# Optimization experiments

Hardware: AMD Instinct MI355X
Metric: run time of the kernel (lower is better)

The kernel has to match this reference:

```python
import jax, jax.numpy as jnp
import numpy as np

B, S, D = 2, 2048, 1024
H, DK, DV = 16, 64, 64
LN_EPS = 1e-5

def setup_inputs() -> dict:
    key = jax.random.key(0)
    ks = jax.random.split(key, 12)
    f = lambda k, shp: jax.random.normal(k, shp, dtype=jnp.float32)
    causal = jnp.triu(jnp.ones((S, S), dtype=jnp.bool_), k=1)  # True = masked
    return {
        'Q': f(ks[0], (B, S, D)),
        'K': f(ks[1], (B, S, D)),
        'V': f(ks[2], (B, S, D)),
        'attention_mask': jnp.broadcast_to(causal, (B, S, S)),
        'WQ_w': f(ks[3], (D, H * DK)) * 0.02, 'WQ_b': jnp.zeros((H * DK,), jnp.float32),
        'WK_w': f(ks[4], (D, H * DK)) * 0.02, 'WK_b': jnp.zeros((H * DK,), jnp.float32),
        'WV_w': f(ks[5], (H * DV, D)) * 0.02, 'WV_b': jnp.zeros((D,), jnp.float32),
        'lin_w': f(ks[6], (H * DV, D)) * 0.02, 'lin_b': jnp.zeros((D,), jnp.float32),
        'ln_g': jnp.ones((D,), jnp.float32), 'ln_b': jnp.zeros((D,), jnp.float32),
    }

def reference(Q, K, V, attention_mask, WQ_w, WQ_b, WK_w, WK_b, WV_w, WV_b, lin_w, lin_b, ln_g, ln_b):
    b = Q.shape[0]
    # projections -> (B, H, S, d)
    q = (Q @ WQ_w + WQ_b).reshape(b, -1, H, DK).transpose(0, 2, 1, 3)
    k = (K @ WK_w + WK_b).reshape(b, -1, H, DK).transpose(0, 2, 1, 3)
    v = (V @ WV_w + WV_b).reshape(b, -1, H, DV).transpose(0, 2, 1, 3)
    scale = 1.0 / jnp.sqrt(jnp.asarray(DK, Q.dtype))
    scores = jnp.einsum('bhqd,bhkd->bhqk', q, k) * scale  # (B,H,S,S)
    scores = jnp.where(attention_mask[:, None, :, :], -jnp.inf, scores)
    probs = jax.nn.softmax(scores, axis=-1)
    ctx = jnp.einsum('bhqk,bhkd->bhqd', probs, v)  # attention_weights in original
    ctx2 = ctx.transpose(0, 2, 1, 3).reshape(b, -1, H * DV)  # (B,S,H*DV)
    out = ctx2 @ lin_w + lin_b  # output projection
    res = out + Q
    mu = jnp.mean(res, axis=-1, keepdims=True)
    var = jnp.mean(jnp.square(res - mu), axis=-1, keepdims=True)
    y = (res - mu) * jax.lax.rsqrt(var + LN_EPS) * ln_g + ln_b
    return (y, ctx)
```

## Files before the change

### kernel.cpp

```cpp
#include <hip/hip_runtime.h>
#include <hip/hip_bf16.h>
#include <stdint.h>


typedef __attribute__((ext_vector_type(4))) float  f32x4;
typedef __attribute__((ext_vector_type(8))) __bf16 bf16x8;
typedef __attribute__((ext_vector_type(4))) __bf16 bf16x4;
typedef __attribute__((ext_vector_type(4))) short  short4v;

static constexpr int S_LEN = 2048;
static constexpr int D_MODEL = 1024;
static constexpr int HN = 16;

__device__ __forceinline__ void gload_lds16(const __bf16* g, __bf16* l) {
  __builtin_amdgcn_global_load_lds(
      (const __attribute__((address_space(1))) void*)g,
      (__attribute__((address_space(3))) void*)l, 16, 0, 0);
}

__global__ __launch_bounds__(256) void cvt3(
    const float* __restrict__ a, const float* __restrict__ b, const float* __restrict__ c,
    __bf16* __restrict__ oa, __bf16* __restrict__ ob, __bf16* __restrict__ oc) {
  const float* s = blockIdx.y == 0 ? a : blockIdx.y == 1 ? b : c;
  __bf16* d      = blockIdx.y == 0 ? oa : blockIdx.y == 1 ? ob : oc;
  size_t i = (size_t)blockIdx.x * 256 + threadIdx.x;
  float4 v = ((const float4*)s)[i];
  bf16x4 o;
  o[0] = (__bf16)v.x; o[1] = (__bf16)v.y; o[2] = (__bf16)v.z; o[3] = (__bf16)v.w;
  ((bf16x4*)d)[i] = o;
}

__global__ __launch_bounds__(256) void transpose_cvt(
    const float* __restrict__ s0, const float* __restrict__ s1,
    const float* __restrict__ s2, const float* __restrict__ s3,
    __bf16* __restrict__ d0, __bf16* __restrict__ d1,
    __bf16* __restrict__ d2, __bf16* __restrict__ d3) {
  const float* src = blockIdx.z == 0 ? s0 : blockIdx.z == 1 ? s1 : blockIdx.z == 2 ? s2 : s3;
  __bf16* dst      = blockIdx.z == 0 ? d0 : blockIdx.z == 1 ? d1 : blockIdx.z == 2 ? d2 : d3;
  const int N = 1024;
  __shared__ float tile[32][33];
  const int bx = blockIdx.x * 32, by = blockIdx.y * 32;
  const int tx = threadIdx.x & 31, ty = threadIdx.x >> 5;
#pragma unroll
  for (int r = ty; r < 32; r += 8) tile[r][tx] = src[(size_t)(by + r) * N + bx + tx];
  __syncthreads();
#pragma unroll
  for (int r = ty; r < 32; r += 8) dst[(size_t)(bx + r) * N + by + tx] = (__bf16)tile[tx][r];
}

template <bool SWAP>
__device__ __forceinline__ void gemm128_core(
    const __bf16* __restrict__ A, const __bf16* __restrict__ Bt,
    __bf16* lA, __bf16* lB, int m0, int n0, int tid, f32x4 (&acc)[4][4]) {
  constexpr int K = 1024;
  const int w = tid >> 6, l = tid & 63;
  const int lr = l & 15, q4 = l >> 4;
  const int wm = (w >> 1) * 64, wn = (w & 1) * 64;
  const int srow = l >> 2;
  const int scol = (l & 3) * 8;

  for (int k0 = 0; k0 < K; k0 += 32) {
    __syncthreads();
#pragma unroll
    for (int i = 0; i < 2; i++) {
      const int chunk = w * 2 + i;
      gload_lds16(A  + (size_t)(m0 + chunk * 16 + srow) * K + k0 + scol, &lA[chunk * 512]);
      gload_lds16(Bt + (size_t)(n0 + chunk * 16 + srow) * K + k0 + scol, &lB[chunk * 512]);
    }
    __syncthreads();
    bf16x8 af[4], bfr[4];
#pragma unroll
    for (int mt = 0; mt < 4; mt++)
      af[mt] = *(const bf16x8*)&lA[(wm + mt * 16 + lr) * 32 + q4 * 8];
#pragma unroll
    for (int nt = 0; nt < 4; nt++)
      bfr[nt] = *(const bf16x8*)&lB[(wn + nt * 16 + lr) * 32 + q4 * 8];
#pragma unroll
    for (int mt = 0; mt < 4; mt++)
#pragma unroll
      for (int nt = 0; nt < 4; nt++)
        acc[mt][nt] = SWAP
          ? __builtin_amdgcn_mfma_f32_16x16x32_bf16(bfr[nt], af[mt], acc[mt][nt], 0, 0, 0)
          : __builtin_amdgcn_mfma_f32_16x16x32_bf16(af[mt], bfr[nt], acc[mt][nt], 0, 0, 0);
  }
}

__global__ __launch_bounds__(256) void gemm_qkv(
    const __bf16* __restrict__ Xq, const __bf16* __restrict__ Xk, const __bf16* __restrict__ Xv,
    const __bf16* __restrict__ WqT, const __bf16* __restrict__ WkT, const __bf16* __restrict__ WvT,
    const float* __restrict__ bq, const float* __restrict__ bk, const float* __restrict__ bv,
    __bf16* __restrict__ oq, __bf16* __restrict__ okk, __bf16* __restrict__ ov) {
  const int p = blockIdx.z;
  const __bf16* A    = p == 0 ? Xq  : p == 1 ? Xk  : Xv;
  const __bf16* Bt   = p == 0 ? WqT : p == 1 ? WkT : WvT;
  const float*  bias = p == 0 ? bq  : p == 1 ? bk  : bv;
  __bf16* out        = p == 0 ? oq  : p == 1 ? okk : ov;
  const float scale  = p == 0 ? 0.18033688f : 1.0f;

  const int m0 = blockIdx.x * 128;
  const int n0 = blockIdx.y * 128;

  __shared__ __align__(16) __bf16 lA[128 * 32];
  __shared__ __align__(16) __bf16 lB[128 * 32];

  const int tid = threadIdx.x;
  const int w = tid >> 6, l = tid & 63;
  const int lr = l & 15, q4 = l >> 4;
  const int wm = (w >> 1) * 64, wn = (w & 1) * 64;

  f32x4 acc[4][4] = {};

  if (p == 2) {
    gemm128_core<false>(A, Bt, lA, lB, m0, n0, tid, acc);
#pragma unroll
    for (int nt = 0; nt < 4; nt++) {
      const int n = n0 + wn + nt * 16 + lr;
      const float bs = bias[n];
      const int h = n >> 6, dk = n & 63;
#pragma unroll
      for (int mt = 0; mt < 4; mt++) {
        const int m = m0 + wm + mt * 16 + q4 * 4;
        const int b = m >> 11, sr = m & 2047;
        f32x4 a = acc[mt][nt];
        bf16x4 ob;
        ob[0] = (__bf16)(a[0] + bs); ob[1] = (__bf16)(a[1] + bs);
        ob[2] = (__bf16)(a[2] + bs); ob[3] = (__bf16)(a[3] + bs);
        *(bf16x4*)&out[((size_t)((b * HN + h) * 64 + dk)) * S_LEN + sr] = ob;
      }
    }
  } else {
    gemm128_core<true>(A, Bt, lA, lB, m0, n0, tid, acc);
#pragma unroll
    for (int mt = 0; mt < 4; mt++) {
      const int m = m0 + wm + mt * 16 + lr;
      const int b = m >> 11, sr = m & 2047;
#pragma unroll
      for (int nt = 0; nt < 4; nt++) {
        const int n = n0 + wn + nt * 16 + q4 * 4;
        const int h = n >> 6, dk = n & 63;
        const float4 bs = *(const float4*)&bias[n];
        f32x4 a = acc[mt][nt];
        bf16x4 ob;
        ob[0] = (__bf16)((a[0] + bs.x) * scale); ob[1] = (__bf16)((a[1] + bs.y) * scale);
        ob[2] = (__bf16)((a[2] + bs.z) * scale); ob[3] = (__bf16)((a[3] + bs.w) * scale);
        *(bf16x4*)&out[((size_t)((b * HN + h) * S_LEN + sr)) * 64 + dk] = ob;
      }
    }
  }
}

__global__ __launch_bounds__(256) void gemm_out(
    const __bf16* __restrict__ A, const __bf16* __restrict__ Bt,
    const float* __restrict__ bias, const float* __restrict__ resid,
    float* __restrict__ out) {
  constexpr int K = 1024;
  const int m0 = blockIdx.x * 64;
  const int n0 = blockIdx.y * 128;

  __shared__ __align__(16) __bf16 lA[64 * 32];
  __shared__ __align__(16) __bf16 lB[128 * 32];

  const int tid = threadIdx.x;
  const int w = tid >> 6, l = tid & 63;
  const int lr = l & 15, q4 = l >> 4;
  const int wm = (w >> 1) * 32, wn = (w & 1) * 64;
  const int srow = l >> 2;
  const int scol = (l & 3) * 8;

  f32x4 acc[2][4] = {};

  for (int k0 = 0; k0 < K; k0 += 32) {
    __syncthreads();
    gload_lds16(A + (size_t)(m0 + w * 16 + srow) * K + k0 + scol, &lA[w * 512]);
#pragma unroll
    for (int i = 0; i < 2; i++) {
      const int chunk = w * 2 + i;
      gload_lds16(Bt + (size_t)(n0 + chunk * 16 + srow) * K + k0 + scol, &lB[chunk * 512]);
    }
    __syncthreads();
    bf16x8 af[2], bfr[4];
#pragma unroll
    for (int mt = 0; mt < 2; mt++)
      af[mt] = *(const bf16x8*)&lA[(wm + mt * 16 + lr) * 32 + q4 * 8];
#pragma unroll
    for (int nt = 0; nt < 4; nt++)
      bfr[nt] = *(const bf16x8*)&lB[(wn + nt * 16 + lr) * 32 + q4 * 8];
#pragma unroll
    for (int mt = 0; mt < 2; mt++)
#pragma unroll
      for (int nt = 0; nt < 4; nt++)
        acc[mt][nt] = __builtin_amdgcn_mfma_f32_16x16x32_bf16(bfr[nt], af[mt], acc[mt][nt], 0, 0, 0);
  }

#pragma unroll
  for (int mt = 0; mt < 2; mt++) {
    const int m = m0 + wm + mt * 16 + lr;
#pragma unroll
    for (int nt = 0; nt < 4; nt++) {
      const int n = n0 + wn + nt * 16 + q4 * 4;
      const float4 bs = *(const float4*)&bias[n];
      const float4 rs = *(const float4*)&resid[(size_t)m * D_MODEL + n];
      f32x4 a = acc[mt][nt];
      float4 o = {a[0] + bs.x + rs.x, a[1] + bs.y + rs.y,
                  a[2] + bs.z + rs.z, a[3] + bs.w + rs.w};
      *(float4*)&out[(size_t)m * D_MODEL + n] = o;
    }
  }
}

template <bool DIAG>
__device__ __forceinline__ void attn_tile(
    const __bf16* KLc, const __bf16* VLc, const bf16x8 (&qf)[2][2],
    f32x4 (&Of)[2][4], float (&lsum)[2], int lr, int q4, int w) {
  const int ntU = DIAG ? 2 * w + 2 : 8;

  f32x4 Sf[2][8] = {};
  bf16x8 kf[8][2];
#pragma unroll
  for (int nt = 0; nt < 8; nt++)
    if (nt < ntU) {
#pragma unroll
      for (int ks = 0; ks < 2; ks++)
        kf[nt][ks] = *(const bf16x8*)&KLc[(nt * 16 + lr) * 64 +
                                          (((ks * 4 + q4) ^ (lr & 7)) << 3)];
    }
#pragma unroll
  for (int nt = 0; nt < 8; nt++)
    if (nt < ntU) {
#pragma unroll
      for (int mt = 0; mt < 2; mt++) {
        Sf[mt][nt] = __builtin_amdgcn_mfma_f32_16x16x32_bf16(kf[nt][0], qf[mt][0], Sf[mt][nt], 0, 0, 0);
        Sf[mt][nt] = __builtin_amdgcn_mfma_f32_16x16x32_bf16(kf[nt][1], qf[mt][1], Sf[mt][nt], 0, 0, 0);
      }
    }

  short4v pks[2][8];
#pragma unroll
  for (int nt = 0; nt < 8; nt++)
    if (nt < ntU) {
#pragma unroll
      for (int mt = 0; mt < 2; mt++) {
        f32x4 p;
#pragma unroll
        for (int r = 0; r < 4; r++) {
          float e = __builtin_amdgcn_exp2f(Sf[mt][nt][r]);
          if (DIAG) {
            const int keyl = nt * 16 + q4 * 4 + r;
            const int rowl = w * 32 + mt * 16 + lr;
            if (keyl > rowl) e = 0.0f;
          }
          p[r] = e;
          lsum[mt] += e;
        }
        bf16x4 pk;
        pk[0] = (__bf16)p[0]; pk[1] = (__bf16)p[1];
        pk[2] = (__bf16)p[2]; pk[3] = (__bf16)p[3];
        pks[mt][nt] = __builtin_bit_cast(short4v, pk);
      }
    }

#pragma unroll
  for (int h = 0; h < 2; h++) {
    bf16x4 vf[4][4];
#pragma unroll
    for (int ntl = 0; ntl < 4; ntl++) {
      const int nt = h * 4 + ntl;
      if (nt < ntU) {
#pragma unroll
        for (int dt = 0; dt < 4; dt++)
          vf[ntl][dt] = *(const bf16x4*)&VLc[(dt * 16 + lr) * 128 +
                                             ((((nt * 2 + (q4 >> 1)) ^ lr) << 3) + ((q4 & 1) << 2))];
      }
    }
#pragma unroll
    for (int ntl = 0; ntl < 4; ntl++) {
      const int nt = h * 4 + ntl;
      if (nt < ntU) {
#pragma unroll
        for (int dt = 0; dt < 4; dt++) {
#pragma unroll
          for (int mt = 0; mt < 2; mt++)
            Of[mt][dt] = __builtin_amdgcn_mfma_f32_16x16x16bf16_1k(
                __builtin_bit_cast(short4v, vf[ntl][dt]), pks[mt][nt], Of[mt][dt], 0, 0, 0);
        }
      }
    }
  }
}

__global__ __launch_bounds__(256, 2) void attn(
    const __bf16* __restrict__ qp, const __bf16* __restrict__ kp, const __bf16* __restrict__ vt,
    float* __restrict__ ctxo, __bf16* __restrict__ ctx2) {
  const int lid = blockIdx.x;
  const int bh  = ((lid & 7) << 2) | ((lid >> 3) & 3);
  const int qt  = 15 - (lid >> 5);
  const int tid = threadIdx.x;
  const int l = tid & 63, w = tid >> 6;
  const int lr = l & 15, q4 = l >> 4;
  const size_t base = (size_t)bh * (S_LEN * 64);
  const int qrow0 = qt * 128 + w * 32;

  __shared__ __align__(16) __bf16 KL[2 * 8192];
  __shared__ __align__(16) __bf16 VL[2 * 8192];

  bf16x8 qf[2][2];
#pragma unroll
  for (int mt = 0; mt < 2; mt++)
#pragma unroll
    for (int ks = 0; ks < 2; ks++)
      qf[mt][ks] = *(const bf16x8*)&qp[base + (size_t)(qrow0 + mt * 16 + lr) * 64 + ks * 32 + q4 * 8];

  f32x4 Of[2][4] = {};
  float lsum[2] = {0.0f, 0.0f};

  auto stage = [&](int kt, int b) {
    const int kb = kt * 128;
    const __bf16* ksrc = kp + base + (size_t)kb * 64;
    const __bf16* vsrc = vt + base + kb;
    __bf16* KD = KL + b * 8192;
    __bf16* VD = VL + b * 8192;
#pragma unroll
    for (int j = 0; j < 4; j++) {
      const int g = j * 256 + tid;
      const int r = g >> 3, cs = g & 7;
      gload_lds16(ksrc + (size_t)r * 64 + ((cs ^ (r & 7)) << 3), &KD[g * 8]);
    }
#pragma unroll
    for (int j = 0; j < 4; j++) {
      const int g = j * 256 + tid;
      const int dv = g >> 4, cs = g & 15;
      gload_lds16(vsrc + (size_t)dv * S_LEN + ((cs ^ (dv & 15)) << 3), &VD[g * 8]);
    }
  };

  const int nkt = qt + 1;
  stage(0, 0);
  for (int kt = 0; kt < nkt; kt++) {
    __syncthreads();
    if (kt + 1 < nkt) stage(kt + 1, (kt + 1) & 1);
    const __bf16* KLc = KL + (kt & 1) * 8192;
    const __bf16* VLc = VL + (kt & 1) * 8192;
    if (kt + 1 < nkt)
      attn_tile<false>(KLc, VLc, qf, Of, lsum, lr, q4, w);
    else
      attn_tile<true>(KLc, VLc, qf, Of, lsum, lr, q4, w);
  }

  const int b = bh >> 4, h = bh & 15;
#pragma unroll
  for (int mt = 0; mt < 2; mt++) {
    float v = lsum[mt];
    v += __shfl_xor(v, 16);
    v += __shfl_xor(v, 32);
    const float inv = 1.0f / v;
    const int row = qrow0 + mt * 16 + lr;
#pragma unroll
    for (int dt = 0; dt < 4; dt++) {
      f32x4 o = Of[mt][dt];
      float4 of = {o[0] * inv, o[1] * inv, o[2] * inv, o[3] * inv};
      *(float4*)&ctxo[base + (size_t)row * 64 + dt * 16 + q4 * 4] = of;
      bf16x4 ob;
      ob[0] = (__bf16)of.x; ob[1] = (__bf16)of.y; ob[2] = (__bf16)of.z; ob[3] = (__bf16)of.w;
      *(bf16x4*)&ctx2[((size_t)(b * S_LEN + row)) * D_MODEL + h * 64 + dt * 16 + q4 * 4] = ob;
    }
  }
}

__global__ __launch_bounds__(256) void ln_k(float* __restrict__ y,
                                            const float* __restrict__ g,
                                            const float* __restrict__ bb) {
  const int row = blockIdx.x;
  float4* rowp = (float4*)(y + (size_t)row * D_MODEL);
  float4 x = rowp[threadIdx.x];
  float s  = x.x + x.y + x.z + x.w;
  float s2 = x.x * x.x + x.y * x.y + x.z * x.z + x.w * x.w;
#pragma unroll
  for (int off = 32; off >= 1; off >>= 1) {
    s  += __shfl_xor(s, off);
    s2 += __shfl_xor(s2, off);
  }
  __shared__ float red[8];
  const int w = threadIdx.x >> 6, l = threadIdx.x & 63;
  if (l == 0) { red[w] = s; red[4 + w] = s2; }
  __syncthreads();
  s  = red[0] + red[1] + red[2] + red[3];
  s2 = red[4] + red[5] + red[6] + red[7];
  const float mu  = s * (1.0f / D_MODEL);
  const float var = s2 * (1.0f / D_MODEL) - mu * mu;
  const float rs = rsqrtf(var + 1e-5f);
  float4 gg = ((const float4*)g)[threadIdx.x];
  float4 bv = ((const float4*)bb)[threadIdx.x];
  float4 o;
  o.x = (x.x - mu) * rs * gg.x + bv.x;
  o.y = (x.y - mu) * rs * gg.y + bv.y;
  o.z = (x.z - mu) * rs * gg.z + bv.z;
  o.w = (x.w - mu) * rs * gg.w + bv.w;
  rowp[threadIdx.x] = o;
}

extern "C" void kernel_launch(void* const* d_in, const int* in_sizes, int n_in,
                              void* d_out, int out_size, void* d_ws, size_t ws_size,
                              hipStream_t stream) {
  const float* Q    = (const float*)d_in[0];
  const float* K    = (const float*)d_in[1];
  const float* V    = (const float*)d_in[2];
  const float* WQw  = (const float*)d_in[4];
  const float* WQb  = (const float*)d_in[5];
  const float* WKw  = (const float*)d_in[6];
  const float* WKb  = (const float*)d_in[7];
  const float* WVw  = (const float*)d_in[8];
  const float* WVb  = (const float*)d_in[9];
  const float* LINw = (const float*)d_in[10];
  const float* LINb = (const float*)d_in[11];
  const float* LNg  = (const float*)d_in[12];
  const float* LNb  = (const float*)d_in[13];

  float* y    = (float*)d_out;
  float* ctxo = y + (size_t)4096 * 1024;

  char* ws = (char*)d_ws;
  const size_t SZA = (size_t)4096 * 1024 * 2;
  const size_t SZW = (size_t)1024 * 1024 * 2;
  __bf16* Qbf  = (__bf16*)(ws);
  __bf16* Kbf  = (__bf16*)(ws + SZA);
  __bf16* Vbf  = (__bf16*)(ws + 2 * SZA);
  __bf16* WqT  = (__bf16*)(ws + 3 * SZA);
  __bf16* WkT  = (__bf16*)(ws + 3 * SZA + SZW);
  __bf16* WvT  = (__bf16*)(ws + 3 * SZA + 2 * SZW);
  __bf16* WlT  = (__bf16*)(ws + 3 * SZA + 3 * SZW);
  __bf16* qp   = (__bf16*)(ws + 3 * SZA + 4 * SZW);
  __bf16* kp   = (__bf16*)(ws + 4 * SZA + 4 * SZW);
  __bf16* vtp  = (__bf16*)(ws + 5 * SZA + 4 * SZW);
  __bf16* ctx2 = Qbf;

  cvt3<<<dim3(4096, 3), 256, 0, stream>>>(Q, K, V, Qbf, Kbf, Vbf);
  transpose_cvt<<<dim3(32, 32, 4), 256, 0, stream>>>(WQw, WKw, WVw, LINw, WqT, WkT, WvT, WlT);
  gemm_qkv<<<dim3(32, 8, 3), 256, 0, stream>>>(Qbf, Kbf, Vbf, WqT, WkT, WvT,
                                               WQb, WKb, WVb, qp, kp, vtp);
  attn<<<dim3(512), 256, 0, stream>>>(qp, kp, vtp, ctxo, ctx2);
  gemm_out<<<dim3(64, 8), 256, 0, stream>>>(ctx2, WlT, LINb, Q, y);
  ln_k<<<4096, 256, 0, stream>>>(y, LNg, LNb);
}
```

Before: 269.4 us.

## Double-buffer LDS tiles in QKV and output projection GEMMs

Both GEMM main loops now use two LDS buffers. The next K-slice is prefetched with global_load_lds while MFMAs run on the current slice, and the loop drops from two barriers per iteration to one. The goal is to hide global-load latency behind matrix compute in the projection GEMMs. LDS use per block doubles, which may lower occupancy, and the overlap depends on the barrier's implicit memory wait landing after the compute.

```diff
diff --git a/kernel.cpp b/kernel.cpp
--- a/kernel.cpp
+++ b/kernel.cpp
@@ -59,22 +59,30 @@
   const int srow = l >> 2;
   const int scol = (l & 3) * 8;
 
+  auto stage = [&](int k0, int b) {
+    __bf16* dA = lA + b * 4096;
+    __bf16* dB = lB + b * 4096;
+#pragma unroll
+    for (int i = 0; i < 2; i++) {
+      const int chunk = w * 2 + i;
+      gload_lds16(A  + (size_t)(m0 + chunk * 16 + srow) * K + k0 + scol, &dA[chunk * 512]);
+      gload_lds16(Bt + (size_t)(n0 + chunk * 16 + srow) * K + k0 + scol, &dB[chunk * 512]);
+    }
+  };
+
+  stage(0, 0);
   for (int k0 = 0; k0 < K; k0 += 32) {
     __syncthreads();
-#pragma unroll
-    for (int i = 0; i < 2; i++) {
-      const int chunk = w * 2 + i;
-      gload_lds16(A  + (size_t)(m0 + chunk * 16 + srow) * K + k0 + scol, &lA[chunk * 512]);
-      gload_lds16(Bt + (size_t)(n0 + chunk * 16 + srow) * K + k0 + scol, &lB[chunk * 512]);
-    }
-    __syncthreads();
+    if (k0 + 32 < K) stage(k0 + 32, ((k0 >> 5) + 1) & 1);
+    const __bf16* cA = lA + ((k0 >> 5) & 1) * 4096;
+    const __bf16* cB = lB + ((k0 >> 5) & 1) * 4096;
     bf16x8 af[4], bfr[4];
 #pragma unroll
     for (int mt = 0; mt < 4; mt++)
-      af[mt] = *(const bf16x8*)&lA[(wm + mt * 16 + lr) * 32 + q4 * 8];
+      af[mt] = *(const bf16x8*)&cA[(wm + mt * 16 + lr) * 32 + q4 * 8];
 #pragma unroll
     for (int nt = 0; nt < 4; nt++)
-      bfr[nt] = *(const bf16x8*)&lB[(wn + nt * 16 + lr) * 32 + q4 * 8];
+      bfr[nt] = *(const bf16x8*)&cB[(wn + nt * 16 + lr) * 32 + q4 * 8];
 #pragma unroll
     for (int mt = 0; mt < 4; mt++)
 #pragma unroll
@@ -100,8 +108,8 @@
   const int m0 = blockIdx.x * 128;
   const int n0 = blockIdx.y * 128;
 
-  __shared__ __align__(16) __bf16 lA[128 * 32];
-  __shared__ __align__(16) __bf16 lB[128 * 32];
+  __shared__ __align__(16) __bf16 lA[2 * 4096];
+  __shared__ __align__(16) __bf16 lB[2 * 4096];
 
   const int tid = threadIdx.x;
   const int w = tid >> 6, l = tid & 63;
@@ -157,8 +165,8 @@
   const int m0 = blockIdx.x * 64;
   const int n0 = blockIdx.y * 128;
 
-  __shared__ __align__(16) __bf16 lA[64 * 32];
-  __shared__ __align__(16) __bf16 lB[128 * 32];
+  __shared__ __align__(16) __bf16 lA[2 * 2048];
+  __shared__ __align__(16) __bf16 lB[2 * 4096];
 
   const int tid = threadIdx.x;
   const int w = tid >> 6, l = tid & 63;
@@ -169,22 +177,28 @@
 
   f32x4 acc[2][4] = {};
 
+  auto stage = [&](int k0, int b) {
+    gload_lds16(A + (size_t)(m0 + w * 16 + srow) * K + k0 + scol, &lA[b * 2048 + w * 512]);
+#pragma unroll
+    for (int i = 0; i < 2; i++) {
+      const int chunk = w * 2 + i;
+      gload_lds16(Bt + (size_t)(n0 + chunk * 16 + srow) * K + k0 + scol, &lB[b * 4096 + chunk * 512]);
+    }
+  };
+
+  stage(0, 0);
   for (int k0 = 0; k0 < K; k0 += 32) {
     __syncthreads();
-    gload_lds16(A + (size_t)(m0 + w * 16 + srow) * K + k0 + scol, &lA[w * 512]);
-#pragma unroll
-    for (int i = 0; i < 2; i++) {
-      const int chunk = w * 2 + i;
-      gload_lds16(Bt + (size_t)(n0 + chunk * 16 + srow) * K + k0 + scol, &lB[chunk * 512]);
-    }
-    __syncthreads();
+    if (k0 + 32 < K) stage(k0 + 32, ((k0 >> 5) + 1) & 1);
+    const __bf16* cA = lA + ((k0 >> 5) & 1) * 2048;
+    const __bf16* cB = lB + ((k0 >> 5) & 1) * 4096;
     bf16x8 af[2], bfr[4];
 #pragma unroll
     for (int mt = 0; mt < 2; mt++)
-      af[mt] = *(const bf16x8*)&lA[(wm + mt * 16 + lr) * 32 + q4 * 8];
+      af[mt] = *(const bf16x8*)&cA[(wm + mt * 16 + lr) * 32 + q4 * 8];
 #pragma unroll
     for (int nt = 0; nt < 4; nt++)
-      bfr[nt] = *(const bf16x8*)&lB[(wn + nt * 16 + lr) * 32 + q4 * 8];
+      bfr[nt] = *(const bf16x8*)&cB[(wn + nt * 16 + lr) * 32 + q4 * 8];
 #pragma unroll
     for (int mt = 0; mt < 2; mt++)
 #pragma unroll
```

Result: no change. 269.7 us (+0.1%).
